# Kernel tuning notes

Hardware: AMD Instinct MI355X
Metric: run time of the kernel (lower is better)

## Reference

```python
import jax, jax.numpy as jnp
import numpy as np

B, T, DQ, DV, UNITS = 32, 2048, 1024, 1024, 1024


def setup_inputs() -> dict:
    key = jax.random.key(0)
    ks = jax.random.split(key, 11)
    s_q = 1.0 / np.sqrt(DQ)
    s_v = 1.0 / np.sqrt(DV)
    s_u = 1.0 / np.sqrt(UNITS)
    return {
        "query": jax.random.normal(ks[0], (B, DQ), jnp.float32),
        "values": jax.random.normal(ks[1], (B, T, DV), jnp.float32),
        "prev_coverage": jax.random.uniform(ks[2], (B, T, 1), jnp.float32),
        "Wh": jax.random.normal(ks[3], (DQ, UNITS), jnp.float32) * s_q,
        "bh": jnp.zeros((UNITS,), jnp.float32),
        "Ws": jax.random.normal(ks[4], (DV, UNITS), jnp.float32) * s_v,
        "bs": jnp.zeros((UNITS,), jnp.float32),
        "Wc": jax.random.normal(ks[5], (1, UNITS), jnp.float32),
        "bc": jnp.zeros((UNITS,), jnp.float32),
        "Vw": jax.random.normal(ks[6], (UNITS, 1), jnp.float32) * s_u,
        "Vb": jnp.zeros((1,), jnp.float32),
    }


def reference(query, values, prev_coverage, Wh, bh, Ws, bs, Wc, bc, Vw, Vb):
    # query: [B, DQ] -> [B, 1, UNITS] (broadcast over time)
    q_proj = (query @ Wh + bh)[:, None, :]
    # values: [B, T, DV] -> [B, T, UNITS]
    v_proj = jnp.einsum('btd,du->btu', values, Ws) + bs
    # prev_coverage: [B, T, 1] -> [B, T, UNITS]
    c_proj = prev_coverage * Wc[0] + bc
    # score: [B, T, 1] via inline MLP
    score = jnp.tanh(q_proj + v_proj + c_proj) @ Vw + Vb
    # softmax over time axis (axis=1)
    attention_weights = jax.nn.softmax(score, axis=1)  # [B, T, 1]
    coverage = attention_weights + prev_coverage       # [B, T, 1]
    context_vector = jnp.sum(attention_weights * values, axis=1)  # [B, DV]
    return context_vector, jnp.squeeze(attention_weights, -1), coverage
```

## Files before the change

kernel.cpp:

```cpp
#include <hip/hip_runtime.h>
#include <hip/hip_bf16.h>
#include <stdint.h>

#define NB 32
#define NT 2048
#define ND 1024
#define NU 1024

typedef __attribute__((ext_vector_type(8))) short bf16x8;
typedef __attribute__((ext_vector_type(4))) float f32x4;
typedef __attribute__((ext_vector_type(4))) unsigned short us4;
typedef __attribute__((ext_vector_type(8))) unsigned short us8;

__device__ __forceinline__ unsigned short f2bf(float f) {
  unsigned int u = __float_as_uint(f);
  u = (u + 0x7fffu + ((u >> 16) & 1u)) >> 16;
  return (unsigned short)u;
}

__device__ __forceinline__ float tanh_fast(float x) {
  x = fminf(10.0f, fmaxf(-10.0f, x));
  float t = __expf(2.0f * x);
  return 1.0f - 2.0f * __builtin_amdgcn_rcpf(t + 1.0f);
}

__device__ __forceinline__ void gload_lds16(const void* g, void* s) {
  __builtin_amdgcn_global_load_lds(
      (const __attribute__((address_space(1))) unsigned int*)g,
      (__attribute__((address_space(3))) unsigned int*)s, 16, 0, 0);
}

__global__ void cvt_kernel(const float* __restrict__ v,
                           unsigned short* __restrict__ o) {
  size_t idx = ((size_t)blockIdx.x * 256 + threadIdx.x) * 8;
  const float4* p = (const float4*)(v + idx);
  float4 x = p[0], y = p[1];
  us8 h;
  h[0] = f2bf(x.x); h[1] = f2bf(x.y); h[2] = f2bf(x.z); h[3] = f2bf(x.w);
  h[4] = f2bf(y.x); h[5] = f2bf(y.y); h[6] = f2bf(y.z); h[7] = f2bf(y.w);
  *(us8*)(o + idx) = h;
}

__global__ void wst_kernel(const float* __restrict__ Ws,
                           unsigned short* __restrict__ Wst) {
  __shared__ float tile[32][33];
  int d0 = blockIdx.x * 32, u0 = blockIdx.y * 32;
  int c = threadIdx.x & 31, r8 = threadIdx.x >> 5;
#pragma unroll
  for (int i = 0; i < 4; ++i) {
    int rr = i * 8 + r8;
    tile[rr][c] = Ws[(size_t)(d0 + rr) * NU + u0 + c];
  }
  __syncthreads();
#pragma unroll
  for (int i = 0; i < 4; ++i) {
    int rr = i * 8 + r8;
    Wst[(size_t)(u0 + rr) * ND + d0 + c] = f2bf(tile[c][rr]);
  }
}

__global__ void qb_kernel2(const float* __restrict__ query,
                           const float* __restrict__ Wh,
                           const float* __restrict__ bh,
                           const float* __restrict__ bs,
                           const float* __restrict__ bc,
                           float* __restrict__ qb) {
  int uc = blockIdx.x, b = blockIdx.y;
  int tid = threadIdx.x, ud = tid & 31, ds = tid >> 5;
  const float* q = query + (size_t)b * ND + ds * 128;
  const float4* W4 = (const float4*)Wh + (size_t)ds * 128 * 256 + uc * 32 + ud;
  float4 a = {0.f, 0.f, 0.f, 0.f};
  for (int d = 0; d < 128; ++d) {
    float qv = q[d];
    float4 w = W4[(size_t)d * 256];
    a.x = fmaf(qv, w.x, a.x);
    a.y = fmaf(qv, w.y, a.y);
    a.z = fmaf(qv, w.z, a.z);
    a.w = fmaf(qv, w.w, a.w);
  }
  __shared__ float4 red[8][32];
  red[ds][ud] = a;
  __syncthreads();
  if (tid < 32) {
    float4 s = red[0][tid];
#pragma unroll
    for (int r = 1; r < 8; ++r) {
      float4 t = red[r][tid];
      s.x += t.x; s.y += t.y; s.z += t.z; s.w += t.w;
    }
    int u = uc * 128 + tid * 4;
    s.x += bh[u + 0] + bs[u + 0] + bc[u + 0];
    s.y += bh[u + 1] + bs[u + 1] + bc[u + 1];
    s.z += bh[u + 2] + bs[u + 2] + bc[u + 2];
    s.w += bh[u + 3] + bs[u + 3] + bc[u + 3];
    ((float4*)(qb + (size_t)b * NU))[uc * 32 + tid] = s;
  }
}

__launch_bounds__(256)
__global__ void score_gemm_bf16(const unsigned short* __restrict__ vbf,
                                const unsigned short* __restrict__ Wst,
                                const float* __restrict__ qb,
                                const float* __restrict__ cov,
                                const float* __restrict__ Wc,
                                const float* __restrict__ Vw,
                                float* __restrict__ scores) {
  int bid = blockIdx.x;
  int g  = ((bid >> 6) << 3) | (bid & 7);
  int uc = (bid >> 3) & 7;
  int tc = g & 15;
  int b  = g >> 4;
  const int t0 = tc * 128, u0 = uc * 128;
  const int tid = threadIdx.x;

  __shared__ unsigned short As[128 * 32];
  __shared__ unsigned short Bs[128 * 32];
  __shared__ float covs[128], qbs[128], wcs[128], vws[128];

  if (tid < 128) {
    covs[tid] = cov[(size_t)b * NT + t0 + tid];
    qbs[tid]  = qb[(size_t)b * NU + u0 + tid];
    wcs[tid]  = Wc[u0 + tid];
    vws[tid]  = Vw[u0 + tid];
  }

  f32x4 acc[4][4];
#pragma unroll
  for (int i = 0; i < 4; ++i)
#pragma unroll
    for (int j = 0; j < 4; ++j)
      acc[i][j] = (f32x4){0.f, 0.f, 0.f, 0.f};

  const int lane = tid & 63;
  const int wave = tid >> 6;
  const int wm = wave >> 1, wn = wave & 1;
  const int q = lane >> 4, ln = lane & 15;

  const int Lr = lane >> 2;
  const int cswz = (lane & 3) ^ ((Lr >> 1) & 3);
  const unsigned short* pA0 = vbf + (size_t)(b * NT + t0 + wave * 32 + Lr) * ND + cswz * 8;
  const unsigned short* pA1 = pA0 + (size_t)16 * ND;
  const unsigned short* pB0 = Wst + (size_t)(u0 + wave * 32 + Lr) * ND + cswz * 8;
  const unsigned short* pB1 = pB0 + (size_t)16 * ND;
  unsigned short* sA0 = &As[(wave * 32) * 32];
  unsigned short* sA1 = &As[(wave * 32 + 16) * 32];
  unsigned short* sB0 = &Bs[(wave * 32) * 32];
  unsigned short* sB1 = &Bs[(wave * 32 + 16) * 32];

  const int swz8 = (q ^ ((ln >> 1) & 3)) * 8;
  const unsigned short* aP = &As[(wm * 64 + ln) * 32 + swz8];
  const unsigned short* bP = &Bs[(wn * 64 + ln) * 32 + swz8];

  for (int kk = 0; kk < ND; kk += 32) {
    gload_lds16(pA0, sA0);
    gload_lds16(pA1, sA1);
    gload_lds16(pB0, sB0);
    gload_lds16(pB1, sB1);
    pA0 += 32; pA1 += 32; pB0 += 32; pB1 += 32;
    __syncthreads();

    bf16x8 a[4], bb[4];
#pragma unroll
    for (int i = 0; i < 4; ++i) {
      a[i]  = *(const bf16x8*)(aP + i * 16 * 32);
      bb[i] = *(const bf16x8*)(bP + i * 16 * 32);
    }
#pragma unroll
    for (int i = 0; i < 4; ++i)
#pragma unroll
      for (int j = 0; j < 4; ++j)
        acc[i][j] = __builtin_amdgcn_mfma_f32_16x16x32_bf16(a[i], bb[j], acc[i][j], 0, 0, 0);
    __syncthreads();
  }

  float part[4][4];
#pragma unroll
  for (int tm = 0; tm < 4; ++tm)
#pragma unroll
    for (int r = 0; r < 4; ++r) part[tm][r] = 0.f;

#pragma unroll
  for (int tn = 0; tn < 4; ++tn) {
    int n = wn * 64 + tn * 16 + ln;
    float qv = qbs[n], wc = wcs[n], vw = vws[n];
#pragma unroll
    for (int tm = 0; tm < 4; ++tm) {
#pragma unroll
      for (int r = 0; r < 4; ++r) {
        int m = wm * 64 + tm * 16 + q * 4 + r;
        float pre = acc[tm][tn][r] + qv + covs[m] * wc;
        part[tm][r] += vw * tanh_fast(pre);
      }
    }
  }
#pragma unroll
  for (int tm = 0; tm < 4; ++tm) {
#pragma unroll
    for (int r = 0; r < 4; ++r) {
      float v = part[tm][r];
      v += __shfl_xor(v, 1);
      v += __shfl_xor(v, 2);
      v += __shfl_xor(v, 4);
      v += __shfl_xor(v, 8);
      if (ln == 0) {
        int m = wm * 64 + tm * 16 + q * 4 + r;
        atomicAdd(&scores[(size_t)b * NT + t0 + m], v);
      }
    }
  }
}

__launch_bounds__(256)
__global__ void score_gemm_f32(const float* __restrict__ values,
                               const unsigned short* __restrict__ Wst,
                               const float* __restrict__ qb,
                               const float* __restrict__ cov,
                               const float* __restrict__ Wc,
                               const float* __restrict__ Vw,
                               float* __restrict__ scores) {
  const int uc = blockIdx.x;
  const int tc = blockIdx.y;
  const int b  = blockIdx.z;
  const int t0 = tc * 128, u0 = uc * 128;
  const int tid = threadIdx.x;

  __shared__ unsigned short As[128 * 40];
  __shared__ unsigned short Bs[128 * 40];
  __shared__ float covs[128], qbs[128], wcs[128], vws[128];

  if (tid < 128) {
    covs[tid] = cov[(size_t)b * NT + t0 + tid];
    qbs[tid]  = qb[(size_t)b * NU + u0 + tid];
    wcs[tid]  = Wc[u0 + tid];
    vws[tid]  = Vw[u0 + tid];
  }

  f32x4 acc[4][4];
#pragma unroll
  for (int i = 0; i < 4; ++i)
#pragma unroll
    for (int j = 0; j < 4; ++j)
      acc[i][j] = (f32x4){0.f, 0.f, 0.f, 0.f};

  const int lane = tid & 63;
  const int wave = tid >> 6;
  const int wm = wave >> 1, wn = wave & 1;
  const int q = lane >> 4, ln = lane & 15;

  const int ar = tid >> 3;
  const int ac = (tid & 7) * 4;
  const int brow = tid >> 2;
  const int bcol = (tid & 3) * 8;

  const float* Abase = values + (size_t)(b * NT + t0) * ND;
  const unsigned short* Bbase = Wst + (size_t)u0 * ND;

  for (int kk = 0; kk < ND; kk += 32) {
#pragma unroll
    for (int p = 0; p < 4; ++p) {
      int row = p * 32 + ar;
      float4 v = *(const float4*)(Abase + (size_t)row * ND + kk + ac);
      us4 h;
      h.x = f2bf(v.x); h.y = f2bf(v.y); h.z = f2bf(v.z); h.w = f2bf(v.w);
      *(us4*)&As[row * 40 + ac] = h;
    }
#pragma unroll
    for (int p = 0; p < 2; ++p) {
      int row = p * 64 + brow;
      uint4 v = *(const uint4*)(Bbase + (size_t)row * ND + kk + bcol);
      *(uint4*)&Bs[row * 40 + bcol] = v;
    }
    __syncthreads();

    bf16x8 a[4], bb[4];
#pragma unroll
    for (int i = 0; i < 4; ++i) {
      a[i]  = *(const bf16x8*)&As[(wm * 64 + i * 16 + ln) * 40 + q * 8];
      bb[i] = *(const bf16x8*)&Bs[(wn * 64 + i * 16 + ln) * 40 + q * 8];
    }
#pragma unroll
    for (int i = 0; i < 4; ++i)
#pragma unroll
      for (int j = 0; j < 4; ++j)
        acc[i][j] = __builtin_amdgcn_mfma_f32_16x16x32_bf16(a[i], bb[j], acc[i][j], 0, 0, 0);
    __syncthreads();
  }

  float part[4][4];
#pragma unroll
  for (int tm = 0; tm < 4; ++tm)
#pragma unroll
    for (int r = 0; r < 4; ++r) part[tm][r] = 0.f;

#pragma unroll
  for (int tn = 0; tn < 4; ++tn) {
    int n = wn * 64 + tn * 16 + ln;
    float qv = qbs[n], wc = wcs[n], vw = vws[n];
#pragma unroll
    for (int tm = 0; tm < 4; ++tm) {
#pragma unroll
      for (int r = 0; r < 4; ++r) {
        int m = wm * 64 + tm * 16 + q * 4 + r;
        float pre = acc[tm][tn][r] + qv + covs[m] * wc;
        part[tm][r] += vw * tanh_fast(pre);
      }
    }
  }
#pragma unroll
  for (int tm = 0; tm < 4; ++tm) {
#pragma unroll
    for (int r = 0; r < 4; ++r) {
      float v = part[tm][r];
      v += __shfl_xor(v, 1);
      v += __shfl_xor(v, 2);
      v += __shfl_xor(v, 4);
      v += __shfl_xor(v, 8);
      if (ln == 0) {
        int m = wm * 64 + tm * 16 + q * 4 + r;
        atomicAdd(&scores[(size_t)b * NT + t0 + m], v);
      }
    }
  }
}

__global__ void softmax_fused(const float* __restrict__ scores,
                              const float* __restrict__ cov,
                              float* __restrict__ out) {
  int b = blockIdx.x, tid = threadIdx.x;
  __shared__ float red[4], red2[4];
  const float* s = scores + (size_t)b * NT;
  float m = -1e30f;
  for (int t = tid; t < NT; t += 256) m = fmaxf(m, s[t]);
#pragma unroll
  for (int off = 1; off < 64; off <<= 1) m = fmaxf(m, __shfl_xor(m, off));
  if ((tid & 63) == 0) red[tid >> 6] = m;
  __syncthreads();
  m = fmaxf(fmaxf(red[0], red[1]), fmaxf(red[2], red[3]));
  float l = 0.f;
  for (int t = tid; t < NT; t += 256) l += __expf(s[t] - m);
#pragma unroll
  for (int off = 1; off < 64; off <<= 1) l += __shfl_xor(l, off);
  if ((tid & 63) == 0) red2[tid >> 6] = l;
  __syncthreads();
  float rl = 1.0f / (red2[0] + red2[1] + red2[2] + red2[3]);
  for (int t = tid; t < NT; t += 256) {
    float w = __expf(s[t] - m) * rl;
    size_t idx = (size_t)b * NT + t;
    out[32768 + idx] = w;
    out[98304 + idx] = w + cov[idx];
  }
}

__global__ void context_kernel(const float* __restrict__ values,
                               const float* __restrict__ attn,
                               float* __restrict__ ctx) {
  int b = blockIdx.y, t0 = blockIdx.x * 128, tid = threadIdx.x;
  const float4* v4 = (const float4*)(values + (size_t)b * NT * ND);
  const float* w = attn + (size_t)b * NT + t0;
  float ax = 0.f, ay = 0.f, az = 0.f, aw = 0.f;
  for (int t = 0; t < 128; ++t) {
    float wt = w[t];
    float4 x = v4[(size_t)(t0 + t) * 256 + tid];
    ax = fmaf(wt, x.x, ax);
    ay = fmaf(wt, x.y, ay);
    az = fmaf(wt, x.z, az);
    aw = fmaf(wt, x.w, aw);
  }
  float* c = ctx + (size_t)b * ND + tid * 4;
  atomicAdd(c + 0, ax);
  atomicAdd(c + 1, ay);
  atomicAdd(c + 2, az);
  atomicAdd(c + 3, aw);
}

extern "C" void kernel_launch(void* const* d_in, const int* in_sizes, int n_in,
                              void* d_out, int out_size, void* d_ws, size_t ws_size,
                              hipStream_t stream) {
  (void)in_sizes; (void)n_in; (void)out_size;
  const float* query  = (const float*)d_in[0];
  const float* values = (const float*)d_in[1];
  const float* cov    = (const float*)d_in[2];
  const float* Wh     = (const float*)d_in[3];
  const float* bh     = (const float*)d_in[4];
  const float* Ws     = (const float*)d_in[5];
  const float* bs     = (const float*)d_in[6];
  const float* Wc     = (const float*)d_in[7];
  const float* bc     = (const float*)d_in[8];
  const float* Vw     = (const float*)d_in[9];

  float* out = (float*)d_out;

  const size_t VBF_BYTES = (size_t)NB * NT * ND * 2;
  const size_t need = VBF_BYTES + 2u * 1024 * 1024 + 128u * 1024 + 256u * 1024;
  char* ws = (char*)d_ws;

  if (ws_size >= need) {
    unsigned short* vbf = (unsigned short*)ws;
    unsigned short* Wst = (unsigned short*)(ws + VBF_BYTES);
    float* qb     = (float*)(ws + VBF_BYTES + 2u * 1024 * 1024);
    float* scores = (float*)(ws + VBF_BYTES + 2u * 1024 * 1024 + 128u * 1024);

    hipMemsetAsync(scores, 0, (size_t)NB * NT * sizeof(float), stream);
    hipMemsetAsync(out, 0, (size_t)NB * ND * sizeof(float), stream);

    cvt_kernel<<<32768, 256, 0, stream>>>(values, vbf);
    wst_kernel<<<dim3(32, 32), 256, 0, stream>>>(Ws, Wst);
    qb_kernel2<<<dim3(8, 32), 256, 0, stream>>>(query, Wh, bh, bs, bc, qb);
    score_gemm_bf16<<<4096, 256, 0, stream>>>(vbf, Wst, qb, cov, Wc, Vw, scores);
    softmax_fused<<<NB, 256, 0, stream>>>(scores, cov, out);
    context_kernel<<<dim3(16, 32), 256, 0, stream>>>(values, out + 32768, out);
  } else {
    unsigned short* Wst = (unsigned short*)ws;
    float* qb     = (float*)(ws + 2u * 1024 * 1024);
    float* scores = (float*)(ws + 2u * 1024 * 1024 + 128u * 1024);

    hipMemsetAsync(scores, 0, (size_t)NB * NT * sizeof(float), stream);
    hipMemsetAsync(out, 0, (size_t)NB * ND * sizeof(float), stream);

    wst_kernel<<<dim3(32, 32), 256, 0, stream>>>(Ws, Wst);
    qb_kernel2<<<dim3(8, 32), 256, 0, stream>>>(query, Wh, bh, bs, bc, qb);
    score_gemm_f32<<<dim3(8, 16, 32), 256, 0, stream>>>(values, Wst, qb, cov, Wc, Vw, scores);
    softmax_fused<<<NB, 256, 0, stream>>>(scores, cov, out);
    context_kernel<<<dim3(16, 32), 256, 0, stream>>>(values, out + 32768, out);
  }
}
```

Measured before the change: 635.0 us.

## Fuse prep kernels, fold softmax into score GEMM epilogue, read bf16 values in context

Merges the values conversion, Ws transpose and query projection into one prep launch. The score GEMM now uses a per-tile completion counter so the last block of each time tile computes exp(score) and adds the tile's sum to a per-batch total. The softmax kernel goes away, and the context kernel reads bf16 values instead of fp32, halving that read traffic. The trade-offs: softmax no longer subtracts the max, which risks overflow for large scores; context precision drops; and inter-block atomics plus fences are added.

```diff
diff --git a/kernel.cpp b/kernel.cpp
--- a/kernel.cpp
+++ b/kernel.cpp
@@ -18,6 +18,10 @@
   return (unsigned short)u;
 }
 
+__device__ __forceinline__ float bf2f(unsigned short h) {
+  return __uint_as_float(((unsigned int)h) << 16);
+}
+
 __device__ __forceinline__ float tanh_fast(float x) {
   x = fminf(10.0f, fmaxf(-10.0f, x));
   float t = __expf(2.0f * x);
@@ -30,15 +34,253 @@
       (__attribute__((address_space(3))) unsigned int*)s, 16, 0, 0);
 }
 
-__global__ void cvt_kernel(const float* __restrict__ v,
-                           unsigned short* __restrict__ o) {
-  size_t idx = ((size_t)blockIdx.x * 256 + threadIdx.x) * 8;
-  const float4* p = (const float4*)(v + idx);
-  float4 x = p[0], y = p[1];
-  us8 h;
-  h[0] = f2bf(x.x); h[1] = f2bf(x.y); h[2] = f2bf(x.z); h[3] = f2bf(x.w);
-  h[4] = f2bf(y.x); h[5] = f2bf(y.y); h[6] = f2bf(y.z); h[7] = f2bf(y.w);
-  *(us8*)(o + idx) = h;
+__global__ void prep_kernel(const float* __restrict__ values,
+                            const float* __restrict__ Ws,
+                            const float* __restrict__ query,
+                            const float* __restrict__ Wh,
+                            const float* __restrict__ bh,
+                            const float* __restrict__ bs,
+                            const float* __restrict__ bc,
+                            unsigned short* __restrict__ vbf,
+                            unsigned short* __restrict__ Wst,
+                            float* __restrict__ qb) {
+  int bid = blockIdx.x;
+  int tid = threadIdx.x;
+  if (bid < 256) {
+    int uc = bid & 7, b = bid >> 3;
+    int ud = tid & 31, ds = tid >> 5;
+    const float* q = query + (size_t)b * ND + ds * 128;
+    const float4* W4 = (const float4*)Wh + (size_t)ds * 128 * 256 + uc * 32 + ud;
+    float4 a = {0.f, 0.f, 0.f, 0.f};
+#pragma unroll 4
+    for (int d = 0; d < 128; ++d) {
+      float qv = q[d];
+      float4 w = W4[(size_t)d * 256];
+      a.x = fmaf(qv, w.x, a.x);
+      a.y = fmaf(qv, w.y, a.y);
+      a.z = fmaf(qv, w.z, a.z);
+      a.w = fmaf(qv, w.w, a.w);
+    }
+    __shared__ float4 red[8][32];
+    red[ds][ud] = a;
+    __syncthreads();
+    if (tid < 32) {
+      float4 s = red[0][tid];
+#pragma unroll
+      for (int r = 1; r < 8; ++r) {
+        float4 t = red[r][tid];
+        s.x += t.x; s.y += t.y; s.z += t.z; s.w += t.w;
+      }
+      int u = uc * 128 + tid * 4;
+      s.x += bh[u + 0] + bs[u + 0] + bc[u + 0];
+      s.y += bh[u + 1] + bs[u + 1] + bc[u + 1];
+      s.z += bh[u + 2] + bs[u + 2] + bc[u + 2];
+      s.w += bh[u + 3] + bs[u + 3] + bc[u + 3];
+      ((float4*)(qb + (size_t)b * NU))[uc * 32 + tid] = s;
+    }
+  } else if (bid < 1280) {
+    int b2 = bid - 256;
+    int d0 = (b2 & 31) * 32, u0 = (b2 >> 5) * 32;
+    __shared__ float tile[32][33];
+    int c = tid & 31, r8 = tid >> 5;
+#pragma unroll
+    for (int i = 0; i < 4; ++i) {
+      int rr = i * 8 + r8;
+      tile[rr][c] = Ws[(size_t)(d0 + rr) * NU + u0 + c];
+    }
+    __syncthreads();
+#pragma unroll
+    for (int i = 0; i < 4; ++i) {
+      int rr = i * 8 + r8;
+      Wst[(size_t)(u0 + rr) * ND + d0 + c] = f2bf(tile[c][rr]);
+    }
+  } else {
+    size_t idx = ((size_t)(bid - 1280) * 256 + tid) * 8;
+    const float4* p = (const float4*)(values + idx);
+    float4 x = p[0], y = p[1];
+    us8 h;
+    h[0] = f2bf(x.x); h[1] = f2bf(x.y); h[2] = f2bf(x.z); h[3] = f2bf(x.w);
+    h[4] = f2bf(y.x); h[5] = f2bf(y.y); h[6] = f2bf(y.z); h[7] = f2bf(y.w);
+    *(us8*)(vbf + idx) = h;
+  }
+}
+
+__launch_bounds__(256)
+__global__ void score_gemm_bf16(const unsigned short* __restrict__ vbf,
+                                const unsigned short* __restrict__ Wst,
+                                const float* __restrict__ qb,
+                                const float* __restrict__ cov,
+                                const float* __restrict__ Wc,
+                                const float* __restrict__ Vw,
+                                float* __restrict__ scores,
+                                float* __restrict__ expsc,
+                                float* __restrict__ stats,
+                                int* __restrict__ cnt) {
+  int bid = blockIdx.x;
+  int g  = ((bid >> 6) << 3) | (bid & 7);
+  int uc = (bid >> 3) & 7;
+  int tc = g & 15;
+  int b  = g >> 4;
+  const int t0 = tc * 128, u0 = uc * 128;
+  const int tid = threadIdx.x;
+
+  __shared__ unsigned short As[128 * 32];
+  __shared__ unsigned short Bs[128 * 32];
+  __shared__ float covs[128], qbs[128], wcs[128], vws[128];
+  __shared__ int winner;
+  __shared__ float sred[2];
+
+  if (tid < 128) {
+    covs[tid] = cov[(size_t)b * NT + t0 + tid];
+    qbs[tid]  = qb[(size_t)b * NU + u0 + tid];
+    wcs[tid]  = Wc[u0 + tid];
+    vws[tid]  = Vw[u0 + tid];
+  }
+
+  f32x4 acc[4][4];
+#pragma unroll
+  for (int i = 0; i < 4; ++i)
+#pragma unroll
+    for (int j = 0; j < 4; ++j)
+      acc[i][j] = (f32x4){0.f, 0.f, 0.f, 0.f};
+
+  const int lane = tid & 63;
+  const int wave = tid >> 6;
+  const int wm = wave >> 1, wn = wave & 1;
+  const int q = lane >> 4, ln = lane & 15;
+
+  const int Lr = lane >> 2;
+  const int cswz = (lane & 3) ^ ((Lr >> 1) & 3);
+  const unsigned short* pA0 = vbf + (size_t)(b * NT + t0 + wave * 32 + Lr) * ND + cswz * 8;
+  const unsigned short* pA1 = pA0 + (size_t)16 * ND;
+  const unsigned short* pB0 = Wst + (size_t)(u0 + wave * 32 + Lr) * ND + cswz * 8;
+  const unsigned short* pB1 = pB0 + (size_t)16 * ND;
+  unsigned short* sA0 = &As[(wave * 32) * 32];
+  unsigned short* sA1 = &As[(wave * 32 + 16) * 32];
+  unsigned short* sB0 = &Bs[(wave * 32) * 32];
+  unsigned short* sB1 = &Bs[(wave * 32 + 16) * 32];
+
+  const int swz8 = (q ^ ((ln >> 1) & 3)) * 8;
+  const unsigned short* aP = &As[(wm * 64 + ln) * 32 + swz8];
+  const unsigned short* bP = &Bs[(wn * 64 + ln) * 32 + swz8];
+
+  for (int kk = 0; kk < ND; kk += 32) {
+    gload_lds16(pA0, sA0);
+    gload_lds16(pA1, sA1);
+    gload_lds16(pB0, sB0);
+    gload_lds16(pB1, sB1);
+    pA0 += 32; pA1 += 32; pB0 += 32; pB1 += 32;
+    __syncthreads();
+
+    bf16x8 a[4], bb[4];
+#pragma unroll
+    for (int i = 0; i < 4; ++i) {
+      a[i]  = *(const bf16x8*)(aP + i * 16 * 32);
+      bb[i] = *(const bf16x8*)(bP + i * 16 * 32);
+    }
+#pragma unroll
+    for (int i = 0; i < 4; ++i)
+#pragma unroll
+      for (int j = 0; j < 4; ++j)
+        acc[i][j] = __builtin_amdgcn_mfma_f32_16x16x32_bf16(a[i], bb[j], acc[i][j], 0, 0, 0);
+    __syncthreads();
+  }
+
+  float part[4][4];
+#pragma unroll
+  for (int tm = 0; tm < 4; ++tm)
+#pragma unroll
+    for (int r = 0; r < 4; ++r) part[tm][r] = 0.f;
+
+#pragma unroll
+  for (int tn = 0; tn < 4; ++tn) {
+    int n = wn * 64 + tn * 16 + ln;
+    float qv = qbs[n], wc = wcs[n], vw = vws[n];
+#pragma unroll
+    for (int tm = 0; tm < 4; ++tm) {
+#pragma unroll
+      for (int r = 0; r < 4; ++r) {
+        int m = wm * 64 + tm * 16 + q * 4 + r;
+        float pre = acc[tm][tn][r] + qv + covs[m] * wc;
+        part[tm][r] += vw * tanh_fast(pre);
+      }
+    }
+  }
+#pragma unroll
+  for (int tm = 0; tm < 4; ++tm) {
+#pragma unroll
+    for (int r = 0; r < 4; ++r) {
+      float v = part[tm][r];
+      v += __shfl_xor(v, 1);
+      v += __shfl_xor(v, 2);
+      v += __shfl_xor(v, 4);
+      v += __shfl_xor(v, 8);
+      if (ln == 0) {
+        int m = wm * 64 + tm * 16 + q * 4 + r;
+        atomicAdd(&scores[(size_t)b * NT + t0 + m], v);
+      }
+    }
+  }
+
+  __threadfence();
+  __syncthreads();
+  if (tid == 0) {
+    int old = __hip_atomic_fetch_add(&cnt[b * 16 + tc], 1,
+                                     __ATOMIC_ACQ_REL, __HIP_MEMORY_SCOPE_AGENT);
+    winner = (old == 7) ? 1 : 0;
+  }
+  __syncthreads();
+  if (winner) {
+    __threadfence();
+    if (tid < 128) {
+      float s = __hip_atomic_load(&scores[(size_t)b * NT + t0 + tid],
+                                  __ATOMIC_ACQUIRE, __HIP_MEMORY_SCOPE_AGENT);
+      float e = __expf(s);
+      expsc[(size_t)b * NT + t0 + tid] = e;
+#pragma unroll
+      for (int off = 1; off < 64; off <<= 1) e += __shfl_xor(e, off);
+      if (lane == 0) sred[tid >> 6] = e;
+    }
+    __syncthreads();
+    if (tid == 0) atomicAdd(&stats[b], sred[0] + sred[1]);
+  }
+}
+
+__global__ void context_fused(const unsigned short* __restrict__ vbf,
+                              const float* __restrict__ expsc,
+                              const float* __restrict__ stats,
+                              const float* __restrict__ cov,
+                              float* __restrict__ out) {
+  int tc = blockIdx.x;
+  int b  = blockIdx.y;
+  int tid = threadIdx.x;
+  __shared__ float wsm[128];
+  float rinv = 1.0f / stats[b];
+  int t0 = tc * 128;
+  size_t sbase = (size_t)b * NT + t0;
+  if (tid < 128) {
+    float w = expsc[sbase + tid] * rinv;
+    wsm[tid] = w;
+    out[32768 + sbase + tid] = w;
+    out[98304 + sbase + tid] = w + cov[sbase + tid];
+  }
+  __syncthreads();
+  const unsigned short* vb = vbf + (size_t)(b * NT + t0) * ND + tid * 4;
+  float a0 = 0.f, a1 = 0.f, a2 = 0.f, a3 = 0.f;
+#pragma unroll 4
+  for (int t = 0; t < 128; ++t) {
+    float wt = wsm[t];
+    us4 h = *(const us4*)(vb + (size_t)t * ND);
+    a0 = fmaf(wt, bf2f(h.x), a0);
+    a1 = fmaf(wt, bf2f(h.y), a1);
+    a2 = fmaf(wt, bf2f(h.z), a2);
+    a3 = fmaf(wt, bf2f(h.w), a3);
+  }
+  float* c = out + (size_t)b * ND + tid * 4;
+  atomicAdd(c + 0, a0);
+  atomicAdd(c + 1, a1);
+  atomicAdd(c + 2, a2);
+  atomicAdd(c + 3, a3);
 }
 
 __global__ void wst_kernel(const float* __restrict__ Ws,
@@ -98,119 +340,6 @@
 }
 
 __launch_bounds__(256)
-__global__ void score_gemm_bf16(const unsigned short* __restrict__ vbf,
-                                const unsigned short* __restrict__ Wst,
-                                const float* __restrict__ qb,
-                                const float* __restrict__ cov,
-                                const float* __restrict__ Wc,
-                                const float* __restrict__ Vw,
-                                float* __restrict__ scores) {
-  int bid = blockIdx.x;
-  int g  = ((bid >> 6) << 3) | (bid & 7);
-  int uc = (bid >> 3) & 7;
-  int tc = g & 15;
-  int b  = g >> 4;
-  const int t0 = tc * 128, u0 = uc * 128;
-  const int tid = threadIdx.x;
-
-  __shared__ unsigned short As[128 * 32];
-  __shared__ unsigned short Bs[128 * 32];
-  __shared__ float covs[128], qbs[128], wcs[128], vws[128];
-
-  if (tid < 128) {
-    covs[tid] = cov[(size_t)b * NT + t0 + tid];
-    qbs[tid]  = qb[(size_t)b * NU + u0 + tid];
-    wcs[tid]  = Wc[u0 + tid];
-    vws[tid]  = Vw[u0 + tid];
-  }
-
-  f32x4 acc[4][4];
-#pragma unroll
-  for (int i = 0; i < 4; ++i)
-#pragma unroll
-    for (int j = 0; j < 4; ++j)
-      acc[i][j] = (f32x4){0.f, 0.f, 0.f, 0.f};
-
-  const int lane = tid & 63;
-  const int wave = tid >> 6;
-  const int wm = wave >> 1, wn = wave & 1;
-  const int q = lane >> 4, ln = lane & 15;
-
-  const int Lr = lane >> 2;
-  const int cswz = (lane & 3) ^ ((Lr >> 1) & 3);
-  const unsigned short* pA0 = vbf + (size_t)(b * NT + t0 + wave * 32 + Lr) * ND + cswz * 8;
-  const unsigned short* pA1 = pA0 + (size_t)16 * ND;
-  const unsigned short* pB0 = Wst + (size_t)(u0 + wave * 32 + Lr) * ND + cswz * 8;
-  const unsigned short* pB1 = pB0 + (size_t)16 * ND;
-  unsigned short* sA0 = &As[(wave * 32) * 32];
-  unsigned short* sA1 = &As[(wave * 32 + 16) * 32];
-  unsigned short* sB0 = &Bs[(wave * 32) * 32];
-  unsigned short* sB1 = &Bs[(wave * 32 + 16) * 32];
-
-  const int swz8 = (q ^ ((ln >> 1) & 3)) * 8;
-  const unsigned short* aP = &As[(wm * 64 + ln) * 32 + swz8];
-  const unsigned short* bP = &Bs[(wn * 64 + ln) * 32 + swz8];
-
-  for (int kk = 0; kk < ND; kk += 32) {
-    gload_lds16(pA0, sA0);
-    gload_lds16(pA1, sA1);
-    gload_lds16(pB0, sB0);
-    gload_lds16(pB1, sB1);
-    pA0 += 32; pA1 += 32; pB0 += 32; pB1 += 32;
-    __syncthreads();
-
-    bf16x8 a[4], bb[4];
-#pragma unroll
-    for (int i = 0; i < 4; ++i) {
-      a[i]  = *(const bf16x8*)(aP + i * 16 * 32);
-      bb[i] = *(const bf16x8*)(bP + i * 16 * 32);
-    }
-#pragma unroll
-    for (int i = 0; i < 4; ++i)
-#pragma unroll
-      for (int j = 0; j < 4; ++j)
-        acc[i][j] = __builtin_amdgcn_mfma_f32_16x16x32_bf16(a[i], bb[j], acc[i][j], 0, 0, 0);
-    __syncthreads();
-  }
-
-  float part[4][4];
-#pragma unroll
-  for (int tm = 0; tm < 4; ++tm)
-#pragma unroll
-    for (int r = 0; r < 4; ++r) part[tm][r] = 0.f;
-
-#pragma unroll
-  for (int tn = 0; tn < 4; ++tn) {
-    int n = wn * 64 + tn * 16 + ln;
-    float qv = qbs[n], wc = wcs[n], vw = vws[n];
-#pragma unroll
-    for (int tm = 0; tm < 4; ++tm) {
-#pragma unroll
-      for (int r = 0; r < 4; ++r) {
-        int m = wm * 64 + tm * 16 + q * 4 + r;
-        float pre = acc[tm][tn][r] + qv + covs[m] * wc;
-        part[tm][r] += vw * tanh_fast(pre);
-      }
-    }
-  }
-#pragma unroll
-  for (int tm = 0; tm < 4; ++tm) {
-#pragma unroll
-    for (int r = 0; r < 4; ++r) {
-      float v = part[tm][r];
-      v += __shfl_xor(v, 1);
-      v += __shfl_xor(v, 2);
-      v += __shfl_xor(v, 4);
-      v += __shfl_xor(v, 8);
-      if (ln == 0) {
-        int m = wm * 64 + tm * 16 + q * 4 + r;
-        atomicAdd(&scores[(size_t)b * NT + t0 + m], v);
-      }
-    }
-  }
-}
-
-__launch_bounds__(256)
 __global__ void score_gemm_f32(const float* __restrict__ values,
                                const unsigned short* __restrict__ Wst,
                                const float* __restrict__ qb,
@@ -218,43 +347,30 @@
                                const float* __restrict__ Wc,
                                const float* __restrict__ Vw,
                                float* __restrict__ scores) {
-  const int uc = blockIdx.x;
-  const int tc = blockIdx.y;
-  const int b  = blockIdx.z;
+  const int uc = blockIdx.x, tc = blockIdx.y, b = blockIdx.z;
   const int t0 = tc * 128, u0 = uc * 128;
   const int tid = threadIdx.x;
-
   __shared__ unsigned short As[128 * 40];
   __shared__ unsigned short Bs[128 * 40];
   __shared__ float covs[128], qbs[128], wcs[128], vws[128];
-
   if (tid < 128) {
     covs[tid] = cov[(size_t)b * NT + t0 + tid];
     qbs[tid]  = qb[(size_t)b * NU + u0 + tid];
     wcs[tid]  = Wc[u0 + tid];
     vws[tid]  = Vw[u0 + tid];
   }
-
   f32x4 acc[4][4];
 #pragma unroll
   for (int i = 0; i < 4; ++i)
 #pragma unroll
-    for (int j = 0; j < 4; ++j)
-      acc[i][j] = (f32x4){0.f, 0.f, 0.f, 0.f};
-
-  const int lane = tid & 63;
-  const int wave = tid >> 6;
+    for (int j = 0; j < 4; ++j) acc[i][j] = (f32x4){0.f, 0.f, 0.f, 0.f};
+  const int lane = tid & 63, wave = tid >> 6;
   const int wm = wave >> 1, wn = wave & 1;
   const int q = lane >> 4, ln = lane & 15;
-
-  const int ar = tid >> 3;
-  const int ac = (tid & 7) * 4;
-  const int brow = tid >> 2;
-  const int bcol = (tid & 3) * 8;
-
+  const int ar = tid >> 3, ac = (tid & 7) * 4;
+  const int brow = tid >> 2, bcol = (tid & 3) * 8;
   const float* Abase = values + (size_t)(b * NT + t0) * ND;
   const unsigned short* Bbase = Wst + (size_t)u0 * ND;
-
   for (int kk = 0; kk < ND; kk += 32) {
 #pragma unroll
     for (int p = 0; p < 4; ++p) {
@@ -271,7 +387,6 @@
       *(uint4*)&Bs[row * 40 + bcol] = v;
     }
     __syncthreads();
-
     bf16x8 a[4], bb[4];
 #pragma unroll
     for (int i = 0; i < 4; ++i) {
@@ -285,13 +400,11 @@
         acc[i][j] = __builtin_amdgcn_mfma_f32_16x16x32_bf16(a[i], bb[j], acc[i][j], 0, 0, 0);
     __syncthreads();
   }
-
   float part[4][4];
 #pragma unroll
   for (int tm = 0; tm < 4; ++tm)
 #pragma unroll
     for (int r = 0; r < 4; ++r) part[tm][r] = 0.f;
-
 #pragma unroll
   for (int tn = 0; tn < 4; ++tn) {
     int n = wn * 64 + tn * 16 + ln;
@@ -389,26 +502,34 @@
   const float* Vw     = (const float*)d_in[9];
 
   float* out = (float*)d_out;
-
-  const size_t VBF_BYTES = (size_t)NB * NT * ND * 2;
-  const size_t need = VBF_BYTES + 2u * 1024 * 1024 + 128u * 1024 + 256u * 1024;
   char* ws = (char*)d_ws;
+
+  const size_t VBF = (size_t)NB * NT * ND * 2;
+  const size_t O_WST   = VBF;
+  const size_t O_QB    = O_WST + 2u * 1024 * 1024;
+  const size_t O_SC    = O_QB + 128u * 1024;
+  const size_t O_EXP   = O_SC + 256u * 1024;
+  const size_t O_STATS = O_EXP + 256u * 1024;
+  const size_t O_CNT   = O_STATS + 256;
+  const size_t need    = O_CNT + 2048;
 
   if (ws_size >= need) {
     unsigned short* vbf = (unsigned short*)ws;
-    unsigned short* Wst = (unsigned short*)(ws + VBF_BYTES);
-    float* qb     = (float*)(ws + VBF_BYTES + 2u * 1024 * 1024);
-    float* scores = (float*)(ws + VBF_BYTES + 2u * 1024 * 1024 + 128u * 1024);
-
-    hipMemsetAsync(scores, 0, (size_t)NB * NT * sizeof(float), stream);
+    unsigned short* Wst = (unsigned short*)(ws + O_WST);
+    float* qb     = (float*)(ws + O_QB);
+    float* scores = (float*)(ws + O_SC);
+    float* expsc  = (float*)(ws + O_EXP);
+    float* stats  = (float*)(ws + O_STATS);
+    int*   cnt    = (int*)(ws + O_CNT);
+
+    hipMemsetAsync(scores, 0, need - O_SC, stream);
     hipMemsetAsync(out, 0, (size_t)NB * ND * sizeof(float), stream);
 
-    cvt_kernel<<<32768, 256, 0, stream>>>(values, vbf);
-    wst_kernel<<<dim3(32, 32), 256, 0, stream>>>(Ws, Wst);
-    qb_kernel2<<<dim3(8, 32), 256, 0, stream>>>(query, Wh, bh, bs, bc, qb);
-    score_gemm_bf16<<<4096, 256, 0, stream>>>(vbf, Wst, qb, cov, Wc, Vw, scores);
-    softmax_fused<<<NB, 256, 0, stream>>>(scores, cov, out);
-    context_kernel<<<dim3(16, 32), 256, 0, stream>>>(values, out + 32768, out);
+    prep_kernel<<<34048, 256, 0, stream>>>(values, Ws, query, Wh, bh, bs, bc,
+                                           vbf, Wst, qb);
+    score_gemm_bf16<<<4096, 256, 0, stream>>>(vbf, Wst, qb, cov, Wc, Vw,
+                                              scores, expsc, stats, cnt);
+    context_fused<<<dim3(16, 32), 256, 0, stream>>>(vbf, expsc, stats, cov, out);
   } else {
     unsigned short* Wst = (unsigned short*)ws;
     float* qb     = (float*)(ws + 2u * 1024 * 1024);
```

Result: slower. 959.2 us (+51.1%).
